# Kernel tuning notes

Hardware: AMD Instinct MI355X
Metric: run time of the kernel (lower is better)

Reference implementation:

```python
import jax, jax.numpy as jnp
import numpy as np

B, T, D = 2, 2048, 1024
H, HD = 16, 64
DL, DC = 512, 256
THETA = 10000.0
LN_EPS = 1e-5


def setup_inputs() -> dict:
    key = jax.random.key(0)
    ks = jax.random.split(key, 8)
    s = 0.02
    return {
        "x": jax.random.normal(ks[0], (B, T, D), jnp.float32),
        "W_q": jax.random.normal(ks[1], (H * HD, D), jnp.float32) * s,
        "b_q": jnp.zeros((H * HD,), jnp.float32),
        "W_kvl": jax.random.normal(ks[2], (DL, D), jnp.float32) * s,
        "b_kvl": jnp.zeros((DL,), jnp.float32),
        "ts_scale": jnp.ones((DL,), jnp.float32),
        "ts_shift": jnp.zeros((DL,), jnp.float32),
        "W_comp": jax.random.normal(ks[3], (DC, DL), jnp.float32) * s,
        "W_exp": jax.random.normal(ks[4], (DL, DC), jnp.float32) * s,
        "ln_g": jnp.ones((DC,), jnp.float32),
        "ln_b": jnp.zeros((DC,), jnp.float32),
        "W_fkv": jax.random.normal(ks[5], (2 * H * HD, DL), jnp.float32) * s,
        "b_fkv": jnp.zeros((2 * H * HD,), jnp.float32),
        "W_out": jax.random.normal(ks[6], (D, H * HD), jnp.float32) * s,
        "b_out": jnp.zeros((D,), jnp.float32),
    }


def _rope_tables(t_len):
    inv_freq = 1.0 / (THETA ** (jnp.arange(0, HD, 2, dtype=jnp.float32) / HD))
    pos = jnp.arange(t_len, dtype=jnp.float32)
    freqs = pos[:, None] * inv_freq[None, :]          # [T, HD/2]
    cos = jnp.concatenate([jnp.cos(freqs)] * 2, -1)   # [T, HD]
    sin = jnp.concatenate([jnp.sin(freqs)] * 2, -1)
    return cos[None, None], sin[None, None]           # [1,1,T,HD]


def _rotate_half(z):
    return jnp.concatenate([-z[..., HD // 2:], z[..., :HD // 2]], -1)


def reference(x, W_q, b_q, W_kvl, b_kvl, ts_scale, ts_shift, W_comp, W_exp,
              ln_g, ln_b, W_fkv, b_fkv, W_out, b_out):
    # Q path: [B,T,D] -> [B,H,T,HD]
    q = (jnp.einsum('btd,ed->bte', x, W_q) + b_q).reshape(B, T, H, HD).transpose(0, 2, 1, 3)

    # KV latent + learned KVSplice bottleneck
    kvl = jnp.einsum('btd,ld->btl', x, W_kvl) + b_kvl                 # [B,T,DL]
    xt = kvl * jax.nn.softplus(ts_scale) + ts_shift
    c = jnp.einsum('btl,cl->btc', xt, W_comp)                         # [B,T,DC]
    mu = jnp.mean(c, -1, keepdims=True)
    var = jnp.mean(jnp.square(c - mu), -1, keepdims=True)
    c = (c - mu) * jax.lax.rsqrt(var + LN_EPS) * ln_g + ln_b
    dec = jnp.einsum('btc,lc->btl', c, W_exp)                         # [B,T,DL]

    # Decompress latent to K,V
    kv = jnp.einsum('btl,el->bte', dec, W_fkv) + b_fkv                # [B,T,2*H*HD]
    kv = kv.reshape(B, T, 2, H, HD).transpose(2, 0, 3, 1, 4)          # [2,B,H,T,HD]
    k, v = kv[0], kv[1]

    # RoPE
    cos, sin = _rope_tables(T)
    q = q * cos + _rotate_half(q) * sin
    k = k * cos + _rotate_half(k) * sin

    # Causal SDPA
    scale = 1.0 / np.sqrt(HD)
    scores = jnp.einsum('bhqd,bhkd->bhqk', q, k) * scale
    mask = jnp.tril(jnp.ones((T, T), bool))
    scores = jnp.where(mask, scores, jnp.float32(-1e30))
    attn = jax.nn.softmax(scores, axis=-1)
    o = jnp.einsum('bhqk,bhkd->bhqd', attn, v)
    o = o.transpose(0, 2, 1, 3).reshape(B, T, H * HD)
    return jnp.einsum('bte,de->btd', o, W_out) + b_out
```

## Files before the change

kernel.cpp:

```cpp
#include <hip/hip_runtime.h>
#include <math.h>

#define B_SZ   2
#define T_SEQ  2048
#define NH     16
#define HDIM   64
#define D_MOD  1024
#define DL     512
#define DC     256
#define MROWS  4096

typedef __attribute__((ext_vector_type(8))) short bf16x8;
typedef __attribute__((ext_vector_type(4))) float f32x4;

#define SCALE_Q 0.18033688011112042f

static __device__ __forceinline__ unsigned short f2bf(float f) {
    union { float f; unsigned u; } v; v.f = f;
    unsigned r = v.u + 0x7fffu + ((v.u >> 16) & 1u);
    return (unsigned short)(r >> 16);
}

static __device__ __forceinline__ void gl_lds16(const unsigned short* g,
                                                unsigned short* l) {
    __builtin_amdgcn_global_load_lds(
        (const __attribute__((address_space(1))) unsigned int*)g,
        (__attribute__((address_space(3))) unsigned int*)l, 16, 0, 0);
}

__global__ __launch_bounds__(256) void cvt_bf16(
    const float* __restrict__ x,  const float* __restrict__ wq,
    const float* __restrict__ wkvl, const float* __restrict__ wcomp,
    const float* __restrict__ wexp, const float* __restrict__ wfkv,
    const float* __restrict__ wout,
    unsigned short* __restrict__ xb,  unsigned short* __restrict__ wqh,
    unsigned short* __restrict__ wkvlh, unsigned short* __restrict__ wcomph,
    unsigned short* __restrict__ wexph, unsigned short* __restrict__ wfkvh,
    unsigned short* __restrict__ wouth, float2* __restrict__ rope_tab)
{
    const int g = blockIdx.x * 256 + threadIdx.x;
    const int stride = gridDim.x * 256;
#define CVT_SEG(src, dst, n4)                                              \
    for (int i = g; i < (n4); i += stride) {                               \
        float4 v = ((const float4*)(src))[i];                              \
        unsigned short h[4] = {f2bf(v.x), f2bf(v.y), f2bf(v.z), f2bf(v.w)};\
        *(uint2*)((dst) + (size_t)i * 4) = *(uint2*)h;                     \
    }
    CVT_SEG(x, xb, 1048576)
    CVT_SEG(wq, wqh, 262144)
    CVT_SEG(wkvl, wkvlh, 131072)
    CVT_SEG(wcomp, wcomph, 32768)
    CVT_SEG(wexp, wexph, 32768)
    CVT_SEG(wfkv, wfkvh, 262144)
    CVT_SEG(wout, wouth, 262144)
#undef CVT_SEG
    for (int i = g; i < T_SEQ * 32; i += stride) {
        const int t = i >> 5, fi = i & 31;
        const float inv = __expf((float)fi * (-9.210340371976184f / 32.0f));
        float sn, cs; sincosf((float)t * inv, &sn, &cs);
        rope_tab[i] = make_float2(cs, sn);
    }
}

__global__ __launch_bounds__(256) void gemm_qxt(
    const unsigned short* __restrict__ A, const unsigned short* __restrict__ Wq,
    const unsigned short* __restrict__ Wkvl,
    const float* __restrict__ b_q, const float* __restrict__ b_kvl,
    const float* __restrict__ ts_scale, const float* __restrict__ ts_shift,
    const float2* __restrict__ tab,
    unsigned short* __restrict__ qh, unsigned short* __restrict__ xt)
{
    __shared__ unsigned short As[128 * 32];
    __shared__ unsigned short Ws[128 * 32];

    const int tid = threadIdx.x;
    const int w = tid >> 6, lane = tid & 63;
    const int l16 = lane & 15, quad = lane >> 4;
    const int wm = w >> 1, wn = w & 1;
    const int m0 = blockIdx.x * 128;
    const bool is_q = (blockIdx.y < 8);
    const int n0 = is_q ? blockIdx.y * 128 : (blockIdx.y - 8) * 128;
    const unsigned short* W = is_q ? Wq : Wkvl;
    const int K = D_MOD;

    const int srow = lane >> 2;
    const int scol = (lane & 3) << 3;
    const unsigned short* Ag = A + (size_t)(m0 + w * 32 + srow) * K + scol;
    const unsigned short* Wg = W + (size_t)(n0 + w * 32 + srow) * K + scol;
    unsigned short* Al0 = &As[w * 1024];
    unsigned short* Al1 = &As[w * 1024 + 512];
    unsigned short* Wl0 = &Ws[w * 1024];
    unsigned short* Wl1 = &Ws[w * 1024 + 512];

    f32x4 acc[4][4];
#pragma unroll
    for (int i = 0; i < 4; ++i)
#pragma unroll
        for (int j = 0; j < 4; ++j) acc[i][j] = (f32x4){0.f, 0.f, 0.f, 0.f};

    for (int k0 = 0; k0 < K; k0 += 32) {
        __syncthreads();
        gl_lds16(Ag + k0, Al0);
        gl_lds16(Ag + (size_t)16 * K + k0, Al1);
        gl_lds16(Wg + k0, Wl0);
        gl_lds16(Wg + (size_t)16 * K + k0, Wl1);
        __syncthreads();

        bf16x8 af[4], bfr[4];
#pragma unroll
        for (int i = 0; i < 4; ++i)
            af[i] = *(const bf16x8*)&As[(wm * 64 + i * 16 + l16) * 32 + quad * 8];
#pragma unroll
        for (int j = 0; j < 4; ++j)
            bfr[j] = *(const bf16x8*)&Ws[(wn * 64 + j * 16 + l16) * 32 + quad * 8];
#pragma unroll
        for (int i = 0; i < 4; ++i)
#pragma unroll
            for (int j = 0; j < 4; ++j)
                acc[i][j] = __builtin_amdgcn_mfma_f32_16x16x32_bf16(
                    af[i], bfr[j], acc[i][j], 0, 0, 0);
    }

    if (is_q) {
#pragma unroll
        for (int i = 0; i < 4; ++i) {
#pragma unroll
            for (int j = 0; j < 4; ++j) {
                const int col = n0 + wn * 64 + j * 16 + l16;
                const int h = col >> 6, hd = col & 63;
                const float bv = b_q[col];
                const float bvp = b_q[col ^ 32];
                const float sgn = (hd < 32) ? -1.f : 1.f;
#pragma unroll
                for (int reg = 0; reg < 4; ++reg) {
                    const int row = m0 + wm * 64 + i * 16 + quad * 4 + reg;
                    const int b = row >> 11, t = row & (T_SEQ - 1);
                    const float2 cssn = tab[t * 32 + (hd & 31)];
                    const float v  = acc[i][j][reg] + bv;
                    const float vp = acc[i][j ^ 2][reg] + bvp;
                    const float r = (v * cssn.x + sgn * vp * cssn.y) * SCALE_Q;
                    qh[(((size_t)b * NH + h) * T_SEQ + t) * HDIM + hd] = f2bf(r);
                }
            }
        }
    } else {
#pragma unroll
        for (int i = 0; i < 4; ++i) {
#pragma unroll
            for (int j = 0; j < 4; ++j) {
                const int col = n0 + wn * 64 + j * 16 + l16;
                const float bv = b_kvl[col];
                const float sp_s = log1pf(expf(ts_scale[col]));
                const float sp_t = ts_shift[col];
#pragma unroll
                for (int reg = 0; reg < 4; ++reg) {
                    const int row = m0 + wm * 64 + i * 16 + quad * 4 + reg;
                    const float val = (acc[i][j][reg] + bv) * sp_s + sp_t;
                    xt[(size_t)row * DL + col] = f2bf(val);
                }
            }
        }
    }
}

__global__ __launch_bounds__(256) void gemm_kv(
    const unsigned short* __restrict__ A, const unsigned short* __restrict__ W,
    const float* __restrict__ bias, const float2* __restrict__ tab,
    unsigned short* __restrict__ kh, unsigned short* __restrict__ vth)
{
    __shared__ unsigned short As[128 * 32];
    __shared__ unsigned short Ws[128 * 32];

    const int tid = threadIdx.x;
    const int w = tid >> 6, lane = tid & 63;
    const int l16 = lane & 15, quad = lane >> 4;
    const int wm = w >> 1, wn = w & 1;
    const int m0 = blockIdx.x * 128, n0 = blockIdx.y * 128;
    const int K = DL;

    const int srow = lane >> 2;
    const int scol = (lane & 3) << 3;
    const unsigned short* Ag = A + (size_t)(m0 + w * 32 + srow) * K + scol;
    const unsigned short* Wg = W + (size_t)(n0 + w * 32 + srow) * K + scol;
    unsigned short* Al0 = &As[w * 1024];
    unsigned short* Al1 = &As[w * 1024 + 512];
    unsigned short* Wl0 = &Ws[w * 1024];
    unsigned short* Wl1 = &Ws[w * 1024 + 512];

    f32x4 acc[4][4];
#pragma unroll
    for (int i = 0; i < 4; ++i)
#pragma unroll
        for (int j = 0; j < 4; ++j) acc[i][j] = (f32x4){0.f, 0.f, 0.f, 0.f};

    for (int k0 = 0; k0 < K; k0 += 32) {
        __syncthreads();
        gl_lds16(Ag + k0, Al0);
        gl_lds16(Ag + (size_t)16 * K + k0, Al1);
        gl_lds16(Wg + k0, Wl0);
        gl_lds16(Wg + (size_t)16 * K + k0, Wl1);
        __syncthreads();

        bf16x8 af[4], bfr[4];
#pragma unroll
        for (int i = 0; i < 4; ++i)
            af[i] = *(const bf16x8*)&As[(wm * 64 + i * 16 + l16) * 32 + quad * 8];
#pragma unroll
        for (int j = 0; j < 4; ++j)
            bfr[j] = *(const bf16x8*)&Ws[(wn * 64 + j * 16 + l16) * 32 + quad * 8];
#pragma unroll
        for (int i = 0; i < 4; ++i)
#pragma unroll
            for (int j = 0; j < 4; ++j)
                acc[i][j] = __builtin_amdgcn_mfma_f32_16x16x32_bf16(
                    af[i], bfr[j], acc[i][j], 0, 0, 0);
    }

    if (n0 < 1024) {
#pragma unroll
        for (int i = 0; i < 4; ++i) {
#pragma unroll
            for (int j = 0; j < 4; ++j) {
                const int col = n0 + wn * 64 + j * 16 + l16;
                const int h = (col >> 6) & 15, hd = col & 63;
                const float bv = bias[col];
                const float bvp = bias[col ^ 32];
                const float sgn = (hd < 32) ? -1.f : 1.f;
#pragma unroll
                for (int reg = 0; reg < 4; ++reg) {
                    const int row = m0 + wm * 64 + i * 16 + quad * 4 + reg;
                    const int b = row >> 11, t = row & (T_SEQ - 1);
                    const float2 cssn = tab[t * 32 + (hd & 31)];
                    const float v  = acc[i][j][reg] + bv;
                    const float vp = acc[i][j ^ 2][reg] + bvp;
                    const float r = v * cssn.x + sgn * vp * cssn.y;
                    kh[(((size_t)b * NH + h) * T_SEQ + t) * HDIM + hd] = f2bf(r);
                }
            }
        }
    } else {
#pragma unroll
        for (int i = 0; i < 4; ++i) {
#pragma unroll
            for (int j = 0; j < 4; ++j) {
                const int col = n0 + wn * 64 + j * 16 + l16;
                const int cv = col - 1024;
                const int h = cv >> 6, hd = cv & 63;
                const float bv = bias[col];
                unsigned short hv[4];
                const int r0 = m0 + wm * 64 + i * 16 + quad * 4;
                const int b = r0 >> 11, t0 = r0 & (T_SEQ - 1);
#pragma unroll
                for (int reg = 0; reg < 4; ++reg)
                    hv[reg] = f2bf(acc[i][j][reg] + bv);
                *(uint2*)&vth[(((size_t)b * NH + h) * HDIM + hd) * T_SEQ + t0] =
                    *(uint2*)hv;
            }
        }
    }
}

enum { EP_C = 0, EP_B = 1 };

template <int EPI>
__global__ __launch_bounds__(256) void gemm_mfma64(
    const unsigned short* __restrict__ A, const unsigned short* __restrict__ W,
    void* __restrict__ Cv, int N, int K)
{
    __shared__ unsigned short As[64 * 32];
    __shared__ unsigned short Ws[64 * 32];

    const int tid = threadIdx.x;
    const int w = tid >> 6, lane = tid & 63;
    const int l16 = lane & 15, quad = lane >> 4;
    const int wm = w >> 1, wn = w & 1;
    const int m0 = blockIdx.x * 64, n0 = blockIdx.y * 64;

    const unsigned short* Ag = A + (size_t)(m0 + w * 16 + (lane >> 2)) * K + ((lane & 3) << 3);
    const unsigned short* Wg = W + (size_t)(n0 + w * 16 + (lane >> 2)) * K + ((lane & 3) << 3);
    unsigned short* Al = &As[w * 512];
    unsigned short* Wl = &Ws[w * 512];

    f32x4 acc[2][2];
#pragma unroll
    for (int i = 0; i < 2; ++i)
#pragma unroll
        for (int j = 0; j < 2; ++j) acc[i][j] = (f32x4){0.f, 0.f, 0.f, 0.f};

    for (int k0 = 0; k0 < K; k0 += 32) {
        __syncthreads();
        gl_lds16(Ag + k0, Al);
        gl_lds16(Wg + k0, Wl);
        __syncthreads();

        bf16x8 af[2], bfr[2];
#pragma unroll
        for (int i = 0; i < 2; ++i)
            af[i] = *(const bf16x8*)&As[(wm * 32 + i * 16 + l16) * 32 + quad * 8];
#pragma unroll
        for (int j = 0; j < 2; ++j)
            bfr[j] = *(const bf16x8*)&Ws[(wn * 32 + j * 16 + l16) * 32 + quad * 8];
#pragma unroll
        for (int i = 0; i < 2; ++i)
#pragma unroll
            for (int j = 0; j < 2; ++j)
                acc[i][j] = __builtin_amdgcn_mfma_f32_16x16x32_bf16(
                    af[i], bfr[j], acc[i][j], 0, 0, 0);
    }

#pragma unroll
    for (int i = 0; i < 2; ++i) {
#pragma unroll
        for (int j = 0; j < 2; ++j) {
            const int col = n0 + wn * 32 + j * 16 + l16;
#pragma unroll
            for (int reg = 0; reg < 4; ++reg) {
                const int row = m0 + wm * 32 + i * 16 + quad * 4 + reg;
                if (EPI == EP_C)
                    ((float*)Cv)[(size_t)row * N + col] = acc[i][j][reg];
                else
                    ((unsigned short*)Cv)[(size_t)row * N + col] = f2bf(acc[i][j][reg]);
            }
        }
    }
}

__global__ __launch_bounds__(256) void gemm_out(
    const unsigned short* __restrict__ A, const unsigned short* __restrict__ W,
    const float* __restrict__ bias, float* __restrict__ C, int N, int K)
{
    __shared__ unsigned short As[128 * 32];
    __shared__ unsigned short Ws[128 * 32];

    const int tid = threadIdx.x;
    const int w = tid >> 6, lane = tid & 63;
    const int l16 = lane & 15, quad = lane >> 4;
    const int wm = w >> 1, wn = w & 1;
    const int m0 = blockIdx.x * 128, n0 = blockIdx.y * 128;

    const int srow = lane >> 2;
    const int scol = (lane & 3) << 3;
    const unsigned short* Ag = A + (size_t)(m0 + w * 32 + srow) * K + scol;
    const unsigned short* Wg = W + (size_t)(n0 + w * 32 + srow) * K + scol;
    unsigned short* Al0 = &As[w * 1024];
    unsigned short* Al1 = &As[w * 1024 + 512];
    unsigned short* Wl0 = &Ws[w * 1024];
    unsigned short* Wl1 = &Ws[w * 1024 + 512];

    f32x4 acc[4][4];
#pragma unroll
    for (int i = 0; i < 4; ++i)
#pragma unroll
        for (int j = 0; j < 4; ++j) acc[i][j] = (f32x4){0.f, 0.f, 0.f, 0.f};

    for (int k0 = 0; k0 < K; k0 += 32) {
        __syncthreads();
        gl_lds16(Ag + k0, Al0);
        gl_lds16(Ag + (size_t)16 * K + k0, Al1);
        gl_lds16(Wg + k0, Wl0);
        gl_lds16(Wg + (size_t)16 * K + k0, Wl1);
        __syncthreads();

        bf16x8 af[4], bfr[4];
#pragma unroll
        for (int i = 0; i < 4; ++i)
            af[i] = *(const bf16x8*)&As[(wm * 64 + i * 16 + l16) * 32 + quad * 8];
#pragma unroll
        for (int j = 0; j < 4; ++j)
            bfr[j] = *(const bf16x8*)&Ws[(wn * 64 + j * 16 + l16) * 32 + quad * 8];
#pragma unroll
        for (int i = 0; i < 4; ++i)
#pragma unroll
            for (int j = 0; j < 4; ++j)
                acc[i][j] = __builtin_amdgcn_mfma_f32_16x16x32_bf16(
                    af[i], bfr[j], acc[i][j], 0, 0, 0);
    }

#pragma unroll
    for (int i = 0; i < 4; ++i)
#pragma unroll
        for (int j = 0; j < 4; ++j) {
            const int col = n0 + wn * 64 + j * 16 + l16;
            const float bv = bias[col];
#pragma unroll
            for (int reg = 0; reg < 4; ++reg) {
                const int row = m0 + wm * 64 + i * 16 + quad * 4 + reg;
                C[(size_t)row * N + col] = acc[i][j][reg] + bv;
            }
        }
}

__global__ __launch_bounds__(256) void ln_rows(const float* __restrict__ cbuf,
                                               unsigned short* __restrict__ outb,
                                               const float* __restrict__ g,
                                               const float* __restrict__ bta)
{
    const int row = blockIdx.x, tid = threadIdx.x;
    float v = cbuf[(size_t)row * DC + tid];
    __shared__ float red[8];

    float s = v;
#pragma unroll
    for (int off = 32; off > 0; off >>= 1) s += __shfl_down(s, off);
    if ((tid & 63) == 0) red[tid >> 6] = s;
    __syncthreads();
    const float mu = (red[0] + red[1] + red[2] + red[3]) * (1.0f / DC);

    const float d = v - mu;
    float s2 = d * d;
#pragma unroll
    for (int off = 32; off > 0; off >>= 1) s2 += __shfl_down(s2, off);
    if ((tid & 63) == 0) red[4 + (tid >> 6)] = s2;
    __syncthreads();
    const float var = (red[4] + red[5] + red[6] + red[7]) * (1.0f / DC);

    outb[(size_t)row * DC + tid] = f2bf(d * rsqrtf(var + 1e-5f) * g[tid] + bta[tid]);
}

__global__ __launch_bounds__(256, 3) void flash_mfma(
    const unsigned short* __restrict__ q, const unsigned short* __restrict__ k,
    const unsigned short* __restrict__ vt, unsigned short* __restrict__ o)
{
    __shared__ unsigned short Ks[64 * 72];
    __shared__ unsigned short Vs[64 * 72];
    __shared__ unsigned short Ps[64 * 72];

    const int bh = blockIdx.x & 31;
    const int j  = 31 - (blockIdx.x >> 5);
    const int q0 = j * 64;
    const int tid = threadIdx.x;
    const int w = tid >> 6, lane = tid & 63;
    const int l16 = lane & 15, quad = lane >> 4;
    const int rbase = q0 + w * 16;

    bf16x8 qf[2];
#pragma unroll
    for (int kk = 0; kk < 2; ++kk)
        qf[kk] = *(const bf16x8*)(q + ((size_t)bh * T_SEQ + rbase + l16) * HDIM + kk * 32 + quad * 8);

    f32x4 of[4];
    float lrow[4];
#pragma unroll
    for (int dt = 0; dt < 4; ++dt) of[dt] = (f32x4){0.f, 0.f, 0.f, 0.f};
#pragma unroll
    for (int r = 0; r < 4; ++r) lrow[r] = 0.f;

    const int ldr = tid >> 2;
    const int ldc = (tid & 3) * 16;
    const unsigned short* kgb = k + ((size_t)bh * T_SEQ + ldr) * HDIM + ldc;
    const unsigned short* vgb = vt + ((size_t)bh * HDIM + ldr) * T_SEQ + ldc;

    const int kend = (j + 1) * 64;
    for (int k0 = 0; k0 < kend; k0 += 64) {
        __syncthreads();
        {
            const unsigned short* kg = kgb + (size_t)k0 * HDIM;
            *(bf16x8*)&Ks[ldr * 72 + ldc]     = *(const bf16x8*)kg;
            *(bf16x8*)&Ks[ldr * 72 + ldc + 8] = *(const bf16x8*)(kg + 8);
            const unsigned short* vg = vgb + k0;
            *(bf16x8*)&Vs[ldr * 72 + ldc]     = *(const bf16x8*)vg;
            *(bf16x8*)&Vs[ldr * 72 + ldc + 8] = *(const bf16x8*)(vg + 8);
        }
        __syncthreads();

        bf16x8 kf[4][2];
#pragma unroll
        for (int nt = 0; nt < 4; ++nt)
#pragma unroll
            for (int kk = 0; kk < 2; ++kk)
                kf[nt][kk] = *(const bf16x8*)&Ks[(nt * 16 + l16) * 72 + kk * 32 + quad * 8];

        f32x4 sf[4];
#pragma unroll
        for (int nt = 0; nt < 4; ++nt) {
            sf[nt] = (f32x4){0.f, 0.f, 0.f, 0.f};
#pragma unroll
            for (int kk = 0; kk < 2; ++kk)
                sf[nt] = __builtin_amdgcn_mfma_f32_16x16x32_bf16(qf[kk], kf[nt][kk], sf[nt], 0, 0, 0);
        }

        const bool need_mask = (k0 + 63) > rbase;
#pragma unroll
        for (int reg = 0; reg < 4; ++reg) {
            float a0 = sf[0][reg], a1 = sf[1][reg], a2 = sf[2][reg], a3 = sf[3][reg];
            if (need_mask) {
                const int tq = rbase + quad * 4 + reg;
                if (k0 +      l16 > tq) a0 = -1e30f;
                if (k0 + 16 + l16 > tq) a1 = -1e30f;
                if (k0 + 32 + l16 > tq) a2 = -1e30f;
                if (k0 + 48 + l16 > tq) a3 = -1e30f;
            }
            const float p0 = exp2f(a0), p1 = exp2f(a1);
            const float p2 = exp2f(a2), p3 = exp2f(a3);
            lrow[reg] += (p0 + p1) + (p2 + p3);
            const int prow = (w * 16 + quad * 4 + reg) * 72 + l16;
            Ps[prow]      = f2bf(p0);
            Ps[prow + 16] = f2bf(p1);
            Ps[prow + 32] = f2bf(p2);
            Ps[prow + 48] = f2bf(p3);
        }

        bf16x8 vf[4][2];
#pragma unroll
        for (int dt = 0; dt < 4; ++dt)
#pragma unroll
            for (int kk = 0; kk < 2; ++kk)
                vf[dt][kk] = *(const bf16x8*)&Vs[(dt * 16 + l16) * 72 + kk * 32 + quad * 8];

        bf16x8 pf[2];
#pragma unroll
        for (int kk = 0; kk < 2; ++kk)
            pf[kk] = *(const bf16x8*)&Ps[(w * 16 + l16) * 72 + kk * 32 + quad * 8];
#pragma unroll
        for (int dt = 0; dt < 4; ++dt)
#pragma unroll
            for (int kk = 0; kk < 2; ++kk)
                of[dt] = __builtin_amdgcn_mfma_f32_16x16x32_bf16(pf[kk], vf[dt][kk], of[dt], 0, 0, 0);
    }

    const int b = bh >> 4, h = bh & 15;
#pragma unroll
    for (int reg = 0; reg < 4; ++reg) {
        float l = lrow[reg];
        l += __shfl_xor(l, 1);
        l += __shfl_xor(l, 2);
        l += __shfl_xor(l, 4);
        l += __shfl_xor(l, 8);
        const float inv = 1.0f / l;
        const int t = rbase + quad * 4 + reg;
#pragma unroll
        for (int dt = 0; dt < 4; ++dt)
            o[((size_t)b * T_SEQ + t) * (NH * HDIM) + h * HDIM + dt * 16 + l16] =
                f2bf(of[dt][reg] * inv);
    }
}

extern "C" void kernel_launch(void* const* d_in, const int* in_sizes, int n_in,
                              void* d_out, int out_size, void* d_ws, size_t ws_size,
                              hipStream_t stream)
{
    (void)in_sizes; (void)n_in; (void)out_size; (void)ws_size;

    const float* x        = (const float*)d_in[0];
    const float* W_q      = (const float*)d_in[1];
    const float* b_q      = (const float*)d_in[2];
    const float* W_kvl    = (const float*)d_in[3];
    const float* b_kvl    = (const float*)d_in[4];
    const float* ts_scale = (const float*)d_in[5];
    const float* ts_shift = (const float*)d_in[6];
    const float* W_comp   = (const float*)d_in[7];
    const float* W_exp    = (const float*)d_in[8];
    const float* ln_g     = (const float*)d_in[9];
    const float* ln_b     = (const float*)d_in[10];
    const float* W_fkv    = (const float*)d_in[11];
    const float* b_fkv    = (const float*)d_in[12];
    const float* W_out    = (const float*)d_in[13];
    const float* b_out    = (const float*)d_in[14];
    float* out = (float*)d_out;

    char* p = (char*)d_ws;
    unsigned short* xb     = (unsigned short*)p;             p += 8  * 1024 * 1024;
    unsigned short* wqh    = (unsigned short*)p;             p += 2  * 1024 * 1024;
    unsigned short* wkvlh  = (unsigned short*)p;             p += 1  * 1024 * 1024;
    unsigned short* wcomph = (unsigned short*)p;             p += 256 * 1024;
    unsigned short* wexph  = (unsigned short*)p;             p += 256 * 1024;
    unsigned short* wfkvh  = (unsigned short*)p;             p += 2  * 1024 * 1024;
    unsigned short* wouth  = (unsigned short*)p;             p += 2  * 1024 * 1024;
    unsigned short* qh     = (unsigned short*)p;             p += 8  * 1024 * 1024;
    unsigned short* kh     = (unsigned short*)p;             p += 8  * 1024 * 1024;
    unsigned short* vth    = (unsigned short*)p;             p += 8  * 1024 * 1024;
    unsigned short* xt     = (unsigned short*)p;             p += 4  * 1024 * 1024;
    float*          cb     = (float*)p;                      p += 4  * 1024 * 1024;
    unsigned short* cbh    = (unsigned short*)p;             p += 2  * 1024 * 1024;
    unsigned short* dec    = (unsigned short*)p;             p += 4  * 1024 * 1024;
    unsigned short* ob     = (unsigned short*)p;             p += 8  * 1024 * 1024;
    float2*         tab    = (float2*)p;                     p += 512 * 1024;

    const dim3 blk(256);

    cvt_bf16<<<1024, blk, 0, stream>>>(x, W_q, W_kvl, W_comp, W_exp, W_fkv, W_out,
                                       xb, wqh, wkvlh, wcomph, wexph, wfkvh, wouth,
                                       tab);

    gemm_qxt<<<dim3(32, 12), blk, 0, stream>>>(
        xb, wqh, wkvlh, b_q, b_kvl, ts_scale, ts_shift, tab, qh, xt);

    gemm_mfma64<EP_C><<<dim3(64, 4), blk, 0, stream>>>(
        xt, wcomph, cb, DC, DL);

    ln_rows<<<MROWS, blk, 0, stream>>>(cb, cbh, ln_g, ln_b);

    gemm_mfma64<EP_B><<<dim3(64, 8), blk, 0, stream>>>(
        cbh, wexph, dec, DL, DC);

    gemm_kv<<<dim3(32, 16), blk, 0, stream>>>(
        dec, wfkvh, b_fkv, tab, kh, vth);

    flash_mfma<<<1024, blk, 0, stream>>>(qh, kh, vth, ob);

    gemm_out<<<dim3(32, 8), blk, 0, stream>>>(
        ob, wouth, b_out, out, D_MOD, D_MOD);
}
```

Baseline: 242.2 us.

## Shrink GEMM tiles to 64x128 and restructure flash kernel to two waves

Replaces the three 128x128 projection GEMMs with a shared 64x128 tile macro, doubling grid size so more blocks fill the many compute units. The flash attention kernel now uses 128 threads, each wave handling two 16-row query tiles so K/V fragments loaded from LDS are reused across more rows. It also truncates P to bf16 instead of rounding and accumulates the row sum from the truncated values, which keeps numerator and denominator consistent but adds a little extra truncation error. Smaller GEMM tiles lower per-block reuse and increase global traffic.

```diff
diff --git a/kernel.cpp b/kernel.cpp
--- a/kernel.cpp
+++ b/kernel.cpp
@@ -62,6 +62,40 @@
     }
 }
 
+#define GEMM64x128_PROLOG(Aptr, Wptr, Kdim)                                    \
+    __shared__ unsigned short As[64 * 32];                                     \
+    __shared__ unsigned short Ws[128 * 32];                                    \
+    const int tid = threadIdx.x;                                               \
+    const int w = tid >> 6, lane = tid & 63;                                   \
+    const int l16 = lane & 15, quad = lane >> 4;                               \
+    const int wm = w >> 1, wn = w & 1;                                         \
+    const int srow = lane >> 2, scol = (lane & 3) << 3;                        \
+    const unsigned short* Ag = (Aptr) + (size_t)(m0 + w * 16 + srow) * (Kdim) + scol; \
+    const unsigned short* Wg = (Wptr) + (size_t)(n0 + w * 32 + srow) * (Kdim) + scol; \
+    unsigned short* Al  = &As[w * 512];                                        \
+    unsigned short* Wl0 = &Ws[w * 1024];                                       \
+    unsigned short* Wl1 = &Ws[w * 1024 + 512];                                 \
+    f32x4 acc[2][4];                                                           \
+    _Pragma("unroll") for (int i = 0; i < 2; ++i)                              \
+        _Pragma("unroll") for (int j = 0; j < 4; ++j)                          \
+            acc[i][j] = (f32x4){0.f, 0.f, 0.f, 0.f};                           \
+    for (int k0 = 0; k0 < (Kdim); k0 += 32) {                                  \
+        __syncthreads();                                                       \
+        gl_lds16(Ag + k0, Al);                                                 \
+        gl_lds16(Wg + k0, Wl0);                                                \
+        gl_lds16(Wg + (size_t)16 * (Kdim) + k0, Wl1);                          \
+        __syncthreads();                                                       \
+        bf16x8 af[2], bfr[4];                                                  \
+        _Pragma("unroll") for (int i = 0; i < 2; ++i)                          \
+            af[i] = *(const bf16x8*)&As[(wm * 32 + i * 16 + l16) * 32 + quad * 8]; \
+        _Pragma("unroll") for (int j = 0; j < 4; ++j)                          \
+            bfr[j] = *(const bf16x8*)&Ws[(wn * 64 + j * 16 + l16) * 32 + quad * 8]; \
+        _Pragma("unroll") for (int i = 0; i < 2; ++i)                          \
+            _Pragma("unroll") for (int j = 0; j < 4; ++j)                      \
+                acc[i][j] = __builtin_amdgcn_mfma_f32_16x16x32_bf16(           \
+                    af[i], bfr[j], acc[i][j], 0, 0, 0);                        \
+    }
+
 __global__ __launch_bounds__(256) void gemm_qxt(
     const unsigned short* __restrict__ A, const unsigned short* __restrict__ Wq,
     const unsigned short* __restrict__ Wkvl,
@@ -70,60 +104,16 @@
     const float2* __restrict__ tab,
     unsigned short* __restrict__ qh, unsigned short* __restrict__ xt)
 {
-    __shared__ unsigned short As[128 * 32];
-    __shared__ unsigned short Ws[128 * 32];
-
-    const int tid = threadIdx.x;
-    const int w = tid >> 6, lane = tid & 63;
-    const int l16 = lane & 15, quad = lane >> 4;
-    const int wm = w >> 1, wn = w & 1;
-    const int m0 = blockIdx.x * 128;
+    const int m0 = blockIdx.x * 64;
     const bool is_q = (blockIdx.y < 8);
     const int n0 = is_q ? blockIdx.y * 128 : (blockIdx.y - 8) * 128;
     const unsigned short* W = is_q ? Wq : Wkvl;
-    const int K = D_MOD;
-
-    const int srow = lane >> 2;
-    const int scol = (lane & 3) << 3;
-    const unsigned short* Ag = A + (size_t)(m0 + w * 32 + srow) * K + scol;
-    const unsigned short* Wg = W + (size_t)(n0 + w * 32 + srow) * K + scol;
-    unsigned short* Al0 = &As[w * 1024];
-    unsigned short* Al1 = &As[w * 1024 + 512];
-    unsigned short* Wl0 = &Ws[w * 1024];
-    unsigned short* Wl1 = &Ws[w * 1024 + 512];
-
-    f32x4 acc[4][4];
-#pragma unroll
-    for (int i = 0; i < 4; ++i)
-#pragma unroll
-        for (int j = 0; j < 4; ++j) acc[i][j] = (f32x4){0.f, 0.f, 0.f, 0.f};
-
-    for (int k0 = 0; k0 < K; k0 += 32) {
-        __syncthreads();
-        gl_lds16(Ag + k0, Al0);
-        gl_lds16(Ag + (size_t)16 * K + k0, Al1);
-        gl_lds16(Wg + k0, Wl0);
-        gl_lds16(Wg + (size_t)16 * K + k0, Wl1);
-        __syncthreads();
-
-        bf16x8 af[4], bfr[4];
-#pragma unroll
-        for (int i = 0; i < 4; ++i)
-            af[i] = *(const bf16x8*)&As[(wm * 64 + i * 16 + l16) * 32 + quad * 8];
-#pragma unroll
-        for (int j = 0; j < 4; ++j)
-            bfr[j] = *(const bf16x8*)&Ws[(wn * 64 + j * 16 + l16) * 32 + quad * 8];
-#pragma unroll
-        for (int i = 0; i < 4; ++i)
-#pragma unroll
-            for (int j = 0; j < 4; ++j)
-                acc[i][j] = __builtin_amdgcn_mfma_f32_16x16x32_bf16(
-                    af[i], bfr[j], acc[i][j], 0, 0, 0);
-    }
+
+    GEMM64x128_PROLOG(A, W, D_MOD)
 
     if (is_q) {
 #pragma unroll
-        for (int i = 0; i < 4; ++i) {
+        for (int i = 0; i < 2; ++i) {
 #pragma unroll
             for (int j = 0; j < 4; ++j) {
                 const int col = n0 + wn * 64 + j * 16 + l16;
@@ -133,7 +123,7 @@
                 const float sgn = (hd < 32) ? -1.f : 1.f;
 #pragma unroll
                 for (int reg = 0; reg < 4; ++reg) {
-                    const int row = m0 + wm * 64 + i * 16 + quad * 4 + reg;
+                    const int row = m0 + wm * 32 + i * 16 + quad * 4 + reg;
                     const int b = row >> 11, t = row & (T_SEQ - 1);
                     const float2 cssn = tab[t * 32 + (hd & 31)];
                     const float v  = acc[i][j][reg] + bv;
@@ -145,7 +135,7 @@
         }
     } else {
 #pragma unroll
-        for (int i = 0; i < 4; ++i) {
+        for (int i = 0; i < 2; ++i) {
 #pragma unroll
             for (int j = 0; j < 4; ++j) {
                 const int col = n0 + wn * 64 + j * 16 + l16;
@@ -154,7 +144,7 @@
                 const float sp_t = ts_shift[col];
 #pragma unroll
                 for (int reg = 0; reg < 4; ++reg) {
-                    const int row = m0 + wm * 64 + i * 16 + quad * 4 + reg;
+                    const int row = m0 + wm * 32 + i * 16 + quad * 4 + reg;
                     const float val = (acc[i][j][reg] + bv) * sp_s + sp_t;
                     xt[(size_t)row * DL + col] = f2bf(val);
                 }
@@ -168,57 +158,13 @@
     const float* __restrict__ bias, const float2* __restrict__ tab,
     unsigned short* __restrict__ kh, unsigned short* __restrict__ vth)
 {
-    __shared__ unsigned short As[128 * 32];
-    __shared__ unsigned short Ws[128 * 32];
-
-    const int tid = threadIdx.x;
-    const int w = tid >> 6, lane = tid & 63;
-    const int l16 = lane & 15, quad = lane >> 4;
-    const int wm = w >> 1, wn = w & 1;
-    const int m0 = blockIdx.x * 128, n0 = blockIdx.y * 128;
-    const int K = DL;
-
-    const int srow = lane >> 2;
-    const int scol = (lane & 3) << 3;
-    const unsigned short* Ag = A + (size_t)(m0 + w * 32 + srow) * K + scol;
-    const unsigned short* Wg = W + (size_t)(n0 + w * 32 + srow) * K + scol;
-    unsigned short* Al0 = &As[w * 1024];
-    unsigned short* Al1 = &As[w * 1024 + 512];
-    unsigned short* Wl0 = &Ws[w * 1024];
-    unsigned short* Wl1 = &Ws[w * 1024 + 512];
-
-    f32x4 acc[4][4];
-#pragma unroll
-    for (int i = 0; i < 4; ++i)
-#pragma unroll
-        for (int j = 0; j < 4; ++j) acc[i][j] = (f32x4){0.f, 0.f, 0.f, 0.f};
-
-    for (int k0 = 0; k0 < K; k0 += 32) {
-        __syncthreads();
-        gl_lds16(Ag + k0, Al0);
-        gl_lds16(Ag + (size_t)16 * K + k0, Al1);
-        gl_lds16(Wg + k0, Wl0);
-        gl_lds16(Wg + (size_t)16 * K + k0, Wl1);
-        __syncthreads();
-
-        bf16x8 af[4], bfr[4];
-#pragma unroll
-        for (int i = 0; i < 4; ++i)
-            af[i] = *(const bf16x8*)&As[(wm * 64 + i * 16 + l16) * 32 + quad * 8];
-#pragma unroll
-        for (int j = 0; j < 4; ++j)
-            bfr[j] = *(const bf16x8*)&Ws[(wn * 64 + j * 16 + l16) * 32 + quad * 8];
-#pragma unroll
-        for (int i = 0; i < 4; ++i)
-#pragma unroll
-            for (int j = 0; j < 4; ++j)
-                acc[i][j] = __builtin_amdgcn_mfma_f32_16x16x32_bf16(
-                    af[i], bfr[j], acc[i][j], 0, 0, 0);
-    }
+    const int m0 = blockIdx.x * 64, n0 = blockIdx.y * 128;
+
+    GEMM64x128_PROLOG(A, W, DL)
 
     if (n0 < 1024) {
 #pragma unroll
-        for (int i = 0; i < 4; ++i) {
+        for (int i = 0; i < 2; ++i) {
 #pragma unroll
             for (int j = 0; j < 4; ++j) {
                 const int col = n0 + wn * 64 + j * 16 + l16;
@@ -228,7 +174,7 @@
                 const float sgn = (hd < 32) ? -1.f : 1.f;
 #pragma unroll
                 for (int reg = 0; reg < 4; ++reg) {
-                    const int row = m0 + wm * 64 + i * 16 + quad * 4 + reg;
+                    const int row = m0 + wm * 32 + i * 16 + quad * 4 + reg;
                     const int b = row >> 11, t = row & (T_SEQ - 1);
                     const float2 cssn = tab[t * 32 + (hd & 31)];
                     const float v  = acc[i][j][reg] + bv;
@@ -240,7 +186,7 @@
         }
     } else {
 #pragma unroll
-        for (int i = 0; i < 4; ++i) {
+        for (int i = 0; i < 2; ++i) {
 #pragma unroll
             for (int j = 0; j < 4; ++j) {
                 const int col = n0 + wn * 64 + j * 16 + l16;
@@ -248,7 +194,7 @@
                 const int h = cv >> 6, hd = cv & 63;
                 const float bv = bias[col];
                 unsigned short hv[4];
-                const int r0 = m0 + wm * 64 + i * 16 + quad * 4;
+                const int r0 = m0 + wm * 32 + i * 16 + quad * 4;
                 const int b = r0 >> 11, t0 = r0 & (T_SEQ - 1);
 #pragma unroll
                 for (int reg = 0; reg < 4; ++reg)
@@ -258,6 +204,28 @@
             }
         }
     }
+}
+
+__global__ __launch_bounds__(256) void gemm_out(
+    const unsigned short* __restrict__ A, const unsigned short* __restrict__ W,
+    const float* __restrict__ bias, float* __restrict__ C)
+{
+    const int m0 = blockIdx.x * 64, n0 = blockIdx.y * 128;
+
+    GEMM64x128_PROLOG(A, W, D_MOD)
+
+#pragma unroll
+    for (int i = 0; i < 2; ++i)
+#pragma unroll
+        for (int j = 0; j < 4; ++j) {
+            const int col = n0 + wn * 64 + j * 16 + l16;
+            const float bv = bias[col];
+#pragma unroll
+            for (int reg = 0; reg < 4; ++reg) {
+                const int row = m0 + wm * 32 + i * 16 + quad * 4 + reg;
+                C[(size_t)row * D_MOD + col] = acc[i][j][reg] + bv;
+            }
+        }
 }
 
 enum { EP_C = 0, EP_B = 1 };
@@ -325,71 +293,6 @@
     }
 }
 
-__global__ __launch_bounds__(256) void gemm_out(
-    const unsigned short* __restrict__ A, const unsigned short* __restrict__ W,
-    const float* __restrict__ bias, float* __restrict__ C, int N, int K)
-{
-    __shared__ unsigned short As[128 * 32];
-    __shared__ unsigned short Ws[128 * 32];
-
-    const int tid = threadIdx.x;
-    const int w = tid >> 6, lane = tid & 63;
-    const int l16 = lane & 15, quad = lane >> 4;
-    const int wm = w >> 1, wn = w & 1;
-    const int m0 = blockIdx.x * 128, n0 = blockIdx.y * 128;
-
-    const int srow = lane >> 2;
-    const int scol = (lane & 3) << 3;
-    const unsigned short* Ag = A + (size_t)(m0 + w * 32 + srow) * K + scol;
-    const unsigned short* Wg = W + (size_t)(n0 + w * 32 + srow) * K + scol;
-    unsigned short* Al0 = &As[w * 1024];
-    unsigned short* Al1 = &As[w * 1024 + 512];
-    unsigned short* Wl0 = &Ws[w * 1024];
-    unsigned short* Wl1 = &Ws[w * 1024 + 512];
-
-    f32x4 acc[4][4];
-#pragma unroll
-    for (int i = 0; i < 4; ++i)
-#pragma unroll
-        for (int j = 0; j < 4; ++j) acc[i][j] = (f32x4){0.f, 0.f, 0.f, 0.f};
-
-    for (int k0 = 0; k0 < K; k0 += 32) {
-        __syncthreads();
-        gl_lds16(Ag + k0, Al0);
-        gl_lds16(Ag + (size_t)16 * K + k0, Al1);
-        gl_lds16(Wg + k0, Wl0);
-        gl_lds16(Wg + (size_t)16 * K + k0, Wl1);
-        __syncthreads();
-
-        bf16x8 af[4], bfr[4];
-#pragma unroll
-        for (int i = 0; i < 4; ++i)
-            af[i] = *(const bf16x8*)&As[(wm * 64 + i * 16 + l16) * 32 + quad * 8];
-#pragma unroll
-        for (int j = 0; j < 4; ++j)
-            bfr[j] = *(const bf16x8*)&Ws[(wn * 64 + j * 16 + l16) * 32 + quad * 8];
-#pragma unroll
-        for (int i = 0; i < 4; ++i)
-#pragma unroll
-            for (int j = 0; j < 4; ++j)
-                acc[i][j] = __builtin_amdgcn_mfma_f32_16x16x32_bf16(
-                    af[i], bfr[j], acc[i][j], 0, 0, 0);
-    }
-
-#pragma unroll
-    for (int i = 0; i < 4; ++i)
-#pragma unroll
-        for (int j = 0; j < 4; ++j) {
-            const int col = n0 + wn * 64 + j * 16 + l16;
-            const float bv = bias[col];
-#pragma unroll
-            for (int reg = 0; reg < 4; ++reg) {
-                const int row = m0 + wm * 64 + i * 16 + quad * 4 + reg;
-                C[(size_t)row * N + col] = acc[i][j][reg] + bv;
-            }
-        }
-}
-
 __global__ __launch_bounds__(256) void ln_rows(const float* __restrict__ cbuf,
                                                unsigned short* __restrict__ outb,
                                                const float* __restrict__ g,
@@ -417,7 +320,7 @@
     outb[(size_t)row * DC + tid] = f2bf(d * rsqrtf(var + 1e-5f) * g[tid] + bta[tid]);
 }
 
-__global__ __launch_bounds__(256, 3) void flash_mfma(
+__global__ __launch_bounds__(128) void flash_mfma(
     const unsigned short* __restrict__ q, const unsigned short* __restrict__ k,
     const unsigned short* __restrict__ vt, unsigned short* __restrict__ o)
 {
@@ -431,22 +334,27 @@
     const int tid = threadIdx.x;
     const int w = tid >> 6, lane = tid & 63;
     const int l16 = lane & 15, quad = lane >> 4;
-    const int rbase = q0 + w * 16;
-
-    bf16x8 qf[2];
-#pragma unroll
-    for (int kk = 0; kk < 2; ++kk)
-        qf[kk] = *(const bf16x8*)(q + ((size_t)bh * T_SEQ + rbase + l16) * HDIM + kk * 32 + quad * 8);
-
-    f32x4 of[4];
-    float lrow[4];
-#pragma unroll
-    for (int dt = 0; dt < 4; ++dt) of[dt] = (f32x4){0.f, 0.f, 0.f, 0.f};
-#pragma unroll
-    for (int r = 0; r < 4; ++r) lrow[r] = 0.f;
-
-    const int ldr = tid >> 2;
-    const int ldc = (tid & 3) * 16;
+
+    bf16x8 qf[2][2];
+#pragma unroll
+    for (int mt = 0; mt < 2; ++mt)
+#pragma unroll
+        for (int kk = 0; kk < 2; ++kk)
+            qf[mt][kk] = *(const bf16x8*)(q +
+                ((size_t)bh * T_SEQ + q0 + w * 32 + mt * 16 + l16) * HDIM + kk * 32 + quad * 8);
+
+    f32x4 of[2][4];
+    float lrow[2][4];
+#pragma unroll
+    for (int mt = 0; mt < 2; ++mt) {
+#pragma unroll
+        for (int dt = 0; dt < 4; ++dt) of[mt][dt] = (f32x4){0.f, 0.f, 0.f, 0.f};
+#pragma unroll
+        for (int r = 0; r < 4; ++r) lrow[mt][r] = 0.f;
+    }
+
+    const int ldr = tid >> 1;
+    const int ldc = (tid & 1) * 32;
     const unsigned short* kgb = k + ((size_t)bh * T_SEQ + ldr) * HDIM + ldc;
     const unsigned short* vgb = vt + ((size_t)bh * HDIM + ldr) * T_SEQ + ldc;
 
@@ -455,11 +363,15 @@
         __syncthreads();
         {
             const unsigned short* kg = kgb + (size_t)k0 * HDIM;
-            *(bf16x8*)&Ks[ldr * 72 + ldc]     = *(const bf16x8*)kg;
-            *(bf16x8*)&Ks[ldr * 72 + ldc + 8] = *(const bf16x8*)(kg + 8);
+            *(bf16x8*)&Ks[ldr * 72 + ldc]      = *(const bf16x8*)kg;
+            *(bf16x8*)&Ks[ldr * 72 + ldc + 8]  = *(const bf16x8*)(kg + 8);
+            *(bf16x8*)&Ks[ldr * 72 + ldc + 16] = *(const bf16x8*)(kg + 16);
+            *(bf16x8*)&Ks[ldr * 72 + ldc + 24] = *(const bf16x8*)(kg + 24);
             const unsigned short* vg = vgb + k0;
-            *(bf16x8*)&Vs[ldr * 72 + ldc]     = *(const bf16x8*)vg;
-            *(bf16x8*)&Vs[ldr * 72 + ldc + 8] = *(const bf16x8*)(vg + 8);
+            *(bf16x8*)&Vs[ldr * 72 + ldc]      = *(const bf16x8*)vg;
+            *(bf16x8*)&Vs[ldr * 72 + ldc + 8]  = *(const bf16x8*)(vg + 8);
+            *(bf16x8*)&Vs[ldr * 72 + ldc + 16] = *(const bf16x8*)(vg + 16);
+            *(bf16x8*)&Vs[ldr * 72 + ldc + 24] = *(const bf16x8*)(vg + 24);
         }
         __syncthreads();
 
@@ -470,34 +382,40 @@
             for (int kk = 0; kk < 2; ++kk)
                 kf[nt][kk] = *(const bf16x8*)&Ks[(nt * 16 + l16) * 72 + kk * 32 + quad * 8];
 
-        f32x4 sf[4];
-#pragma unroll
-        for (int nt = 0; nt < 4; ++nt) {
-            sf[nt] = (f32x4){0.f, 0.f, 0.f, 0.f};
-#pragma unroll
-            for (int kk = 0; kk < 2; ++kk)
-                sf[nt] = __builtin_amdgcn_mfma_f32_16x16x32_bf16(qf[kk], kf[nt][kk], sf[nt], 0, 0, 0);
-        }
-
-        const bool need_mask = (k0 + 63) > rbase;
-#pragma unroll
-        for (int reg = 0; reg < 4; ++reg) {
-            float a0 = sf[0][reg], a1 = sf[1][reg], a2 = sf[2][reg], a3 = sf[3][reg];
-            if (need_mask) {
-                const int tq = rbase + quad * 4 + reg;
-                if (k0 +      l16 > tq) a0 = -1e30f;
-                if (k0 + 16 + l16 > tq) a1 = -1e30f;
-                if (k0 + 32 + l16 > tq) a2 = -1e30f;
-                if (k0 + 48 + l16 > tq) a3 = -1e30f;
-            }
-            const float p0 = exp2f(a0), p1 = exp2f(a1);
-            const float p2 = exp2f(a2), p3 = exp2f(a3);
-            lrow[reg] += (p0 + p1) + (p2 + p3);
-            const int prow = (w * 16 + quad * 4 + reg) * 72 + l16;
-            Ps[prow]      = f2bf(p0);
-            Ps[prow + 16] = f2bf(p1);
-            Ps[prow + 32] = f2bf(p2);
-            Ps[prow + 48] = f2bf(p3);
+#pragma unroll
+        for (int mt = 0; mt < 2; ++mt) {
+            const int rbase = q0 + w * 32 + mt * 16;
+            f32x4 sf[4];
+#pragma unroll
+            for (int nt = 0; nt < 4; ++nt) {
+                sf[nt] = (f32x4){0.f, 0.f, 0.f, 0.f};
+#pragma unroll
+                for (int kk = 0; kk < 2; ++kk)
+                    sf[nt] = __builtin_amdgcn_mfma_f32_16x16x32_bf16(qf[mt][kk], kf[nt][kk], sf[nt], 0, 0, 0);
+            }
+            const bool need_mask = (k0 + 63) > rbase;
+#pragma unroll
+            for (int reg = 0; reg < 4; ++reg) {
+                float a0 = sf[0][reg], a1 = sf[1][reg], a2 = sf[2][reg], a3 = sf[3][reg];
+                if (need_mask) {
+                    const int tq = rbase + quad * 4 + reg;
+                    if (k0 +      l16 > tq) a0 = -1e30f;
+                    if (k0 + 16 + l16 > tq) a1 = -1e30f;
+                    if (k0 + 32 + l16 > tq) a2 = -1e30f;
+                    if (k0 + 48 + l16 > tq) a3 = -1e30f;
+                }
+                union { float f; unsigned u; } u0, u1, u2, u3;
+                u0.f = exp2f(a0); u1.f = exp2f(a1);
+                u2.f = exp2f(a2); u3.f = exp2f(a3);
+                const int prow = (w * 32 + mt * 16 + quad * 4 + reg) * 72 + l16;
+                Ps[prow]      = (unsigned short)(u0.u >> 16);
+                Ps[prow + 16] = (unsigned short)(u1.u >> 16);
+                Ps[prow + 32] = (unsigned short)(u2.u >> 16);
+                Ps[prow + 48] = (unsigned short)(u3.u >> 16);
+                u0.u &= 0xffff0000u; u1.u &= 0xffff0000u;
+                u2.u &= 0xffff0000u; u3.u &= 0xffff0000u;
+                lrow[mt][reg] += (u0.f + u1.f) + (u2.f + u3.f);
+            }
         }
 
         bf16x8 vf[4][2];
@@ -507,31 +425,38 @@
             for (int kk = 0; kk < 2; ++kk)
                 vf[dt][kk] = *(const bf16x8*)&Vs[(dt * 16 + l16) * 72 + kk * 32 + quad * 8];
 
-        bf16x8 pf[2];
-#pragma unroll
-        for (int kk = 0; kk < 2; ++kk)
-            pf[kk] = *(const bf16x8*)&Ps[(w * 16 + l16) * 72 + kk * 32 + quad * 8];
-#pragma unroll
-        for (int dt = 0; dt < 4; ++dt)
+#pragma unroll
+        for (int mt = 0; mt < 2; ++mt) {
+            bf16x8 pf[2];
 #pragma unroll
             for (int kk = 0; kk < 2; ++kk)
-                of[dt] = __builtin_amdgcn_mfma_f32_16x16x32_bf16(pf[kk], vf[dt][kk], of[dt], 0, 0, 0);
+                pf[kk] = *(const bf16x8*)&Ps[(w * 32 + mt * 16 + l16) * 72 + kk * 32 + quad * 8];
+#pragma unroll
+            for (int dt = 0; dt < 4; ++dt)
+#pragma unroll
+                for (int kk = 0; kk < 2; ++kk)
+                    of[mt][dt] = __builtin_amdgcn_mfma_f32_16x16x32_bf16(pf[kk], vf[dt][kk], of[mt][dt], 0, 0, 0);
+        }
     }
 
     const int b = bh >> 4, h = bh & 15;
 #pragma unroll
-    for (int reg = 0; reg < 4; ++reg) {
-        float l = lrow[reg];
-        l += __shfl_xor(l, 1);
-        l += __shfl_xor(l, 2);
-        l += __shfl_xor(l, 4);
-        l += __shfl_xor(l, 8);
-        const float inv = 1.0f / l;
-        const int t = rbase + quad * 4 + reg;
-#pragma unroll
-        for (int dt = 0; dt < 4; ++dt)
-            o[((size_t)b * T_SEQ + t) * (NH * HDIM) + h * HDIM + dt * 16 + l16] =
-                f2bf(of[dt][reg] * inv);
+    for (int mt = 0; mt < 2; ++mt) {
+        const int rbase = q0 + w * 32 + mt * 16;
+#pragma unroll
+        for (int reg = 0; reg < 4; ++reg) {
+            float l = lrow[mt][reg];
+            l += __shfl_xor(l, 1);
+            l += __shfl_xor(l, 2);
+            l += __shfl_xor(l, 4);
+            l += __shfl_xor(l, 8);
+            const float inv = 1.0f / l;
+            const int t = rbase + quad * 4 + reg;
+#pragma unroll
+            for (int dt = 0; dt < 4; ++dt)
+                o[((size_t)b * T_SEQ + t) * (NH * HDIM) + h * HDIM + dt * 16 + l16] =
+                    f2bf(of[mt][dt][reg] * inv);
+        }
     }
 }
 
@@ -582,7 +507,7 @@
                                        xb, wqh, wkvlh, wcomph, wexph, wfkvh, wouth,
                                        tab);
 
-    gemm_qxt<<<dim3(32, 12), blk, 0, stream>>>(
+    gemm_qxt<<<dim3(64, 12), blk, 0, stream>>>(
         xb, wqh, wkvlh, b_q, b_kvl, ts_scale, ts_shift, tab, qh, xt);
 
     gemm_mfma64<EP_C><<<dim3(64, 4), blk, 0, stream>>>(
@@ -593,11 +518,11 @@
     gemm_mfma64<EP_B><<<dim3(64, 8), blk, 0, stream>>>(
         cbh, wexph, dec, DL, DC);
 
-    gemm_kv<<<dim3(32, 16), blk, 0, stream>>>(
+    gemm_kv<<<dim3(64, 16), blk, 0, stream>>>(
         dec, wfkvh, b_fkv, tab, kh, vth);
 
-    flash_mfma<<<1024, blk, 0, stream>>>(qh, kh, vth, ob);
-
-    gemm_out<<<dim3(32, 8), blk, 0, stream>>>(
-        ob, wouth, b_out, out, D_MOD, D_MOD);
-}
+    flash_mfma<<<1024, dim3(128), 0, stream>>>(qh, kh, vth, ob);
+
+    gemm_out<<<dim3(64, 8), blk, 0, stream>>>(
+        ob, wouth, b_out, out);
+}
```

Result: slower. 252.2 us (+4.1%).
